# Kernel tuning notes

Measured on AMD Instinct MI355X. Metric: run time of the kernel, lower is better.

## Reference

```python
import jax, jax.numpy as jnp
import numpy as np
import math

# Module hyperparameters (match init_kwargs)
N_LEVELS = 16
LOG2_T = 19
T = 2 ** LOG2_T
BASE = (16, 16)
FINEST = (512, 512)
NUM_HASHGRID = 2
N_POINTS = 1_000_000
PRIME_Y = np.uint32(2654435761)  # standard NGP spatial-hash prime for the 2nd dim


def _resolutions():
    # replicate torch: int(base * b**i) per axis
    b_w = math.exp((math.log(FINEST[0]) - math.log(BASE[0])) / (N_LEVELS - 1))
    b_h = math.exp((math.log(FINEST[1]) - math.log(BASE[1])) / (N_LEVELS - 1))
    res_w = [int(BASE[0] * b_w ** i) for i in range(N_LEVELS)]
    res_h = [int(BASE[1] * b_h ** i) for i in range(N_LEVELS)]
    return jnp.array(np.stack([res_w, res_h], axis=-1), dtype=jnp.int32)  # [L,2]


def setup_inputs() -> dict:
    key = jax.random.key(0)
    k1, k2, k3 = jax.random.split(key, 3)
    x = jax.random.uniform(k1, (N_POINTS, 2), dtype=jnp.float32)
    hash_idxs = jax.random.randint(k2, (N_POINTS, 1), 0, NUM_HASHGRID, dtype=jnp.int32)
    # xavier-normal-like init of the hash tables [G, L, T, F]
    fan_in = N_LEVELS * T * 2
    fan_out = NUM_HASHGRID * T * 2
    std = math.sqrt(2.0 / (fan_in + fan_out))
    features = jax.random.normal(k3, (NUM_HASHGRID, N_LEVELS, T, 2), dtype=jnp.float32) * std
    return {"x": x, "features": features, "hash_idxs": hash_idxs}


def reference(x, features, hash_idxs):
    N = x.shape[0]
    res = _resolutions()                              # [L,2] int32
    scale = (res - 1).astype(jnp.float32)             # [L,2]
    pos = x[:, None, :] * scale[None]                 # [N,L,2]
    i0f = jnp.floor(pos)
    w = pos - i0f                                     # bilinear fractions [N,L,2]
    i0 = i0f.astype(jnp.int32).astype(jnp.uint32)     # [N,L,2]

    # 4 corner offsets: (0,0),(1,0),(0,1),(1,1)
    offs = jnp.array([[0, 0], [1, 0], [0, 1], [1, 1]], dtype=jnp.uint32)  # [4,2]
    corners = i0[:, :, None, :] + offs[None, None]    # [N,L,4,2]
    # NGP spatial hash, modulo table size via mask (T is power of 2)
    h = (corners[..., 0] ^ (corners[..., 1] * PRIME_Y)) & np.uint32(T - 1)  # [N,L,4]
    h = h.astype(jnp.int32)

    g = hash_idxs.reshape(-1)                         # [N] which hash grid
    lidx = jnp.arange(N_LEVELS, dtype=jnp.int32)
    feat = features[g[:, None, None], lidx[None, :, None], h]  # [N,L,4,2]

    wx, wy = w[..., 0], w[..., 1]
    wc = jnp.stack([(1 - wx) * (1 - wy), wx * (1 - wy), (1 - wx) * wy, wx * wy], axis=-1)  # [N,L,4]
    out = jnp.einsum('nlc,nlcf->nlf', wc, feat)       # [N,L,2]
    return out.reshape(N, N_LEVELS * 2)
```

## Files before the change

### kernel.cpp

```cpp
#include <hip/hip_runtime.h>
#include <math.h>

#define NL 16
#define TS (1u << 19)
#define TMASK (TS - 1u)
#define PRIME 2654435761u

#define NBINS 8192
#define BIN_GBIT 12
#define NCOPY 8

struct ScalePack { float s[NL]; };

__device__ __forceinline__ unsigned bin_of(float px, float py, int g) {
    int iy = (int)(py * 511.0f); iy = iy < 0 ? 0 : (iy > 511 ? 511 : iy);
    int ix = (int)(px * 511.0f); ix = ix < 0 ? 0 : (ix > 511 ? 511 : ix);
    return ((unsigned)g << BIN_GBIT) | ((unsigned)iy << 3) | ((unsigned)ix >> 6);
}

__global__ __launch_bounds__(256)
void k_zero(unsigned* __restrict__ p, int n) {
    int i = blockIdx.x * blockDim.x + threadIdx.x;
    if (i < n) p[i] = 0u;
}

__global__ __launch_bounds__(256)
void k_hist8(const float2* __restrict__ x, const int* __restrict__ hidx,
             unsigned* __restrict__ hist, int N)
{
    int n = blockIdx.x * 256 + threadIdx.x;
    if (n >= N) return;
    float2 p = x[n];
    unsigned b = bin_of(p.x, p.y, hidx[n]);
    unsigned c = (unsigned)blockIdx.x & (NCOPY - 1);
    atomicAdd(&hist[c * NBINS + b], 1u);
}

__global__ __launch_bounds__(1024)
void k_scan8(unsigned* __restrict__ hist)
{
    __shared__ unsigned part[1024];
    int t = threadIdx.x;
    int b0 = t * 8;

    unsigned s = 0;
    #pragma unroll
    for (int i = 0; i < 8; ++i) {
        int b = b0 + i;
        #pragma unroll
        for (int c = 0; c < NCOPY; ++c) s += hist[c * NBINS + b];
    }
    part[t] = s;
    __syncthreads();
    for (int d = 1; d < 1024; d <<= 1) {
        unsigned add = (t >= d) ? part[t - d] : 0u;
        __syncthreads();
        part[t] += add;
        __syncthreads();
    }
    unsigned running = t ? part[t - 1] : 0u;

    #pragma unroll
    for (int i = 0; i < 8; ++i) {
        int b = b0 + i;
        unsigned h[NCOPY];
        #pragma unroll
        for (int c = 0; c < NCOPY; ++c) h[c] = hist[c * NBINS + b];
        #pragma unroll
        for (int c = 0; c < NCOPY; ++c) {
            hist[c * NBINS + b] = running;
            running += h[c];
        }
    }
}

__global__ __launch_bounds__(256)
void k_scatter8(const float2* __restrict__ x, const int* __restrict__ hidx,
                unsigned* __restrict__ cur,
                float2* __restrict__ sxy, unsigned* __restrict__ smeta, int N)
{
    int n = blockIdx.x * 256 + threadIdx.x;
    if (n >= N) return;
    float2 p = x[n];
    int g = hidx[n];
    unsigned b = bin_of(p.x, p.y, g);
    unsigned c = (unsigned)blockIdx.x & (NCOPY - 1);
    unsigned pos = atomicAdd(&cur[c * NBINS + b], 1u);
    sxy[pos] = p;
    smeta[pos] = (unsigned)n | ((unsigned)g << 24);
}

__global__ __launch_bounds__(256)
void hashgrid2d_sorted(const float2* __restrict__ sxy,
                       const unsigned* __restrict__ smeta,
                       const float2* __restrict__ feat,
                       float4* __restrict__ out,
                       ScalePack sp, int N)
{
    int nwg = gridDim.x;
    int orig = blockIdx.x;
    int q = nwg >> 3, r = nwg & 7;
    int xcd = orig & 7, loc = orig >> 3;
    int bid = (xcd < r ? xcd * (q + 1) : r * (q + 1) + (xcd - r) * q) + loc;

    int n = bid * 256 + (int)threadIdx.x;
    if (n >= N) return;

    float2 p = sxy[n];
    unsigned meta = smeta[n];
    int g  = (int)(meta >> 24);
    int no = (int)(meta & 0xFFFFFFu);
    float px = p.x, py = p.y;
    const float2* fb = feat + (size_t)g * ((size_t)NL * TS);

    float of[2 * NL];

    #pragma unroll 4
    for (int l = 0; l < NL; ++l) {
        float s  = sp.s[l];
        float fx = px * s;
        float fy = py * s;
        float fx0 = floorf(fx), fy0 = floorf(fy);
        float wx = fx - fx0, wy = fy - fy0;
        unsigned ix = (unsigned)(int)fx0;
        unsigned iy = (unsigned)(int)fy0;
        unsigned hy0 = iy * PRIME;
        unsigned hy1 = (iy + 1u) * PRIME;

        const float2* tab = fb + (size_t)l * TS;
        float2 c00 = tab[( ix       ^ hy0) & TMASK];
        float2 c10 = tab[((ix + 1u) ^ hy0) & TMASK];
        float2 c01 = tab[( ix       ^ hy1) & TMASK];
        float2 c11 = tab[((ix + 1u) ^ hy1) & TMASK];

        float w00 = (1.f - wx) * (1.f - wy);
        float w10 = wx * (1.f - wy);
        float w01 = (1.f - wx) * wy;
        float w11 = wx * wy;

        of[2 * l]     = w00 * c00.x + w10 * c10.x + w01 * c01.x + w11 * c11.x;
        of[2 * l + 1] = w00 * c00.y + w10 * c10.y + w01 * c01.y + w11 * c11.y;
    }

    float4* op = out + (size_t)no * 8;
    #pragma unroll
    for (int qq = 0; qq < 8; ++qq)
        op[qq] = make_float4(of[4 * qq], of[4 * qq + 1], of[4 * qq + 2], of[4 * qq + 3]);
}

__global__ __launch_bounds__(256)
void hashgrid2d_fwd(const float2* __restrict__ x,
                    const float2* __restrict__ feat,
                    const int* __restrict__ hidx,
                    float4* __restrict__ out,
                    ScalePack sp, int N)
{
    int n = blockIdx.x * blockDim.x + threadIdx.x;
    if (n >= N) return;

    float2 p = x[n];
    float px = p.x, py = p.y;
    int g = hidx[n];
    const float2* fb = feat + (size_t)g * ((size_t)NL * TS);

    float of[2 * NL];

    #pragma unroll 4
    for (int l = 0; l < NL; ++l) {
        float s  = sp.s[l];
        float fx = px * s;
        float fy = py * s;
        float fx0 = floorf(fx), fy0 = floorf(fy);
        float wx = fx - fx0, wy = fy - fy0;
        unsigned ix = (unsigned)(int)fx0;
        unsigned iy = (unsigned)(int)fy0;
        unsigned hy0 = iy * PRIME;
        unsigned hy1 = (iy + 1u) * PRIME;

        const float2* tab = fb + (size_t)l * TS;
        float2 c00 = tab[( ix       ^ hy0) & TMASK];
        float2 c10 = tab[((ix + 1u) ^ hy0) & TMASK];
        float2 c01 = tab[( ix       ^ hy1) & TMASK];
        float2 c11 = tab[((ix + 1u) ^ hy1) & TMASK];

        float w00 = (1.f - wx) * (1.f - wy);
        float w10 = wx * (1.f - wy);
        float w01 = (1.f - wx) * wy;
        float w11 = wx * wy;

        of[2 * l]     = w00 * c00.x + w10 * c10.x + w01 * c01.x + w11 * c11.x;
        of[2 * l + 1] = w00 * c00.y + w10 * c10.y + w01 * c01.y + w11 * c11.y;
    }

    float4* op = out + (size_t)n * 8;
    #pragma unroll
    for (int qq = 0; qq < 8; ++qq)
        op[qq] = make_float4(of[4 * qq], of[4 * qq + 1], of[4 * qq + 2], of[4 * qq + 3]);
}

extern "C" void kernel_launch(void* const* d_in, const int* in_sizes, int n_in,
                              void* d_out, int out_size, void* d_ws, size_t ws_size,
                              hipStream_t stream) {
    const float2* x    = (const float2*)d_in[0];
    const float2* feat = (const float2*)d_in[1];
    const int*    hidx = (const int*)d_in[2];
    int N = in_sizes[0] / 2;

    ScalePack sp;
    double b = exp((log(512.0) - log(16.0)) / 15.0);
    for (int i = 0; i < NL; ++i) {
        int r = (int)(16.0 * pow(b, (double)i));
        sp.s[i] = (float)(r - 1);
    }

    int threads = 256;
    int blocks = (N + threads - 1) / threads;

    size_t curB  = (size_t)NCOPY * NBINS * 4;
    size_t xyB   = (size_t)N * 8;
    size_t metaB = (size_t)N * 4;
    size_t need  = curB + xyB + metaB;

    if (d_ws != nullptr && ws_size >= need && N < (1 << 24)) {
        unsigned* cur   = (unsigned*)d_ws;
        float2*   sxy   = (float2*)((char*)d_ws + curB);
        unsigned* smeta = (unsigned*)((char*)d_ws + curB + xyB);

        hipLaunchKernelGGL(k_zero, dim3((NCOPY * NBINS + 255) / 256), dim3(256), 0,
                           stream, cur, NCOPY * NBINS);
        hipLaunchKernelGGL(k_hist8, dim3(blocks), dim3(threads), 0, stream,
                           x, hidx, cur, N);
        hipLaunchKernelGGL(k_scan8, dim3(1), dim3(1024), 0, stream, cur);
        hipLaunchKernelGGL(k_scatter8, dim3(blocks), dim3(threads), 0, stream,
                           x, hidx, cur, sxy, smeta, N);
        hipLaunchKernelGGL(hashgrid2d_sorted, dim3(blocks), dim3(threads), 0, stream,
                           sxy, smeta, feat, (float4*)d_out, sp, N);
    } else {
        hipLaunchKernelGGL(hashgrid2d_fwd, dim3(blocks), dim3(threads), 0, stream,
                           x, feat, hidx, (float4*)d_out, sp, N);
    }
}
```

Measured before the change: 358.0 us.

## Replace global-atomic binning with per-block shared-memory histogram counting sort

Replaces the global-atomic histogram and scatter with a block-local LDS histogram over 256 persistent blocks, a per-bin column scan across blocks, and a global bin-base scan, followed by a scatter that uses LDS atomics. Bins are coarsened from 8192 to 4096. The aim is to cut contention on global atomics and drop the zeroing kernel. The cost is a larger workspace, an extra scan launch, and coarser bins, which may reduce locality in the table gathers. The old path is kept as a fallback when the workspace is too small.

After: 328.0 us. 8.4% less time.

```diff
diff --git a/kernel.cpp b/kernel.cpp
--- a/kernel.cpp
+++ b/kernel.cpp
@@ -6,16 +6,110 @@
 #define TMASK (TS - 1u)
 #define PRIME 2654435761u
 
-#define NBINS 8192
-#define BIN_GBIT 12
+#define SBINS 4096
+#define SBLK  256
+
+#define OBINS 8192
 #define NCOPY 8
 
 struct ScalePack { float s[NL]; };
 
-__device__ __forceinline__ unsigned bin_of(float px, float py, int g) {
+__device__ __forceinline__ unsigned bin4k_of(float px, float py, int g) {
     int iy = (int)(py * 511.0f); iy = iy < 0 ? 0 : (iy > 511 ? 511 : iy);
     int ix = (int)(px * 511.0f); ix = ix < 0 ? 0 : (ix > 511 ? 511 : ix);
-    return ((unsigned)g << BIN_GBIT) | ((unsigned)iy << 3) | ((unsigned)ix >> 6);
+    return ((unsigned)g << 11) | ((unsigned)iy << 2) | ((unsigned)ix >> 7);
+}
+
+__device__ __forceinline__ unsigned bin8k_of(float px, float py, int g) {
+    int iy = (int)(py * 511.0f); iy = iy < 0 ? 0 : (iy > 511 ? 511 : iy);
+    int ix = (int)(px * 511.0f); ix = ix < 0 ? 0 : (ix > 511 ? 511 : ix);
+    return ((unsigned)g << 12) | ((unsigned)iy << 3) | ((unsigned)ix >> 6);
+}
+
+
+__global__ __launch_bounds__(256)
+void k_hist_b(const float2* __restrict__ x, const int* __restrict__ hidx,
+              unsigned* __restrict__ H, int N)
+{
+    __shared__ unsigned lh[SBINS];
+    int t = threadIdx.x;
+    #pragma unroll
+    for (int i = t; i < SBINS; i += 256) lh[i] = 0u;
+    __syncthreads();
+
+    for (int n = blockIdx.x * 256 + t; n < N; n += SBLK * 256) {
+        float2 p = x[n];
+        atomicAdd(&lh[bin4k_of(p.x, p.y, hidx[n])], 1u);
+    }
+    __syncthreads();
+
+    unsigned* row = H + (size_t)blockIdx.x * SBINS;
+    #pragma unroll
+    for (int i = t; i < SBINS; i += 256) row[i] = lh[i];
+}
+
+__global__ __launch_bounds__(256)
+void k_s1(unsigned* __restrict__ H, unsigned* __restrict__ binTotal)
+{
+    __shared__ unsigned part[256];
+    int bin = blockIdx.x;
+    int t = threadIdx.x;
+    unsigned v = H[(size_t)t * SBINS + bin];
+    part[t] = v;
+    __syncthreads();
+    for (int d = 1; d < 256; d <<= 1) {
+        unsigned add = (t >= d) ? part[t - d] : 0u;
+        __syncthreads();
+        part[t] += add;
+        __syncthreads();
+    }
+    unsigned incl = part[t];
+    H[(size_t)t * SBINS + bin] = incl - v;
+    if (t == 255) binTotal[bin] = incl;
+}
+
+__global__ __launch_bounds__(1024)
+void k_s2(const unsigned* __restrict__ binTotal, unsigned* __restrict__ binBase)
+{
+    __shared__ unsigned part[1024];
+    int t = threadIdx.x;
+    unsigned v[4];
+    unsigned s = 0;
+    #pragma unroll
+    for (int i = 0; i < 4; ++i) { v[i] = binTotal[t * 4 + i]; s += v[i]; }
+    part[t] = s;
+    __syncthreads();
+    for (int d = 1; d < 1024; d <<= 1) {
+        unsigned add = (t >= d) ? part[t - d] : 0u;
+        __syncthreads();
+        part[t] += add;
+        __syncthreads();
+    }
+    unsigned base = t ? part[t - 1] : 0u;
+    #pragma unroll
+    for (int i = 0; i < 4; ++i) { binBase[t * 4 + i] = base; base += v[i]; }
+}
+
+__global__ __launch_bounds__(256)
+void k_scatter_b(const float2* __restrict__ x, const int* __restrict__ hidx,
+                 const unsigned* __restrict__ H, const unsigned* __restrict__ binBase,
+                 float2* __restrict__ sxy, unsigned* __restrict__ smeta, int N)
+{
+    __shared__ unsigned cur[SBINS];
+    int t = threadIdx.x;
+    const unsigned* row = H + (size_t)blockIdx.x * SBINS;
+    #pragma unroll
+    for (int i = t; i < SBINS; i += 256) cur[i] = binBase[i] + row[i];
+    __syncthreads();
+
+    for (int n = blockIdx.x * 256 + t; n < N; n += SBLK * 256) {
+        float2 p = x[n];
+        int g = hidx[n];
+        unsigned b = bin4k_of(p.x, p.y, g);
+        unsigned pos = atomicAdd(&cur[b], 1u);
+        sxy[pos] = p;
+        smeta[pos] = (unsigned)n | ((unsigned)g << 24);
+    }
 }
 
 __global__ __launch_bounds__(256)
@@ -31,9 +125,9 @@
     int n = blockIdx.x * 256 + threadIdx.x;
     if (n >= N) return;
     float2 p = x[n];
-    unsigned b = bin_of(p.x, p.y, hidx[n]);
+    unsigned b = bin8k_of(p.x, p.y, hidx[n]);
     unsigned c = (unsigned)blockIdx.x & (NCOPY - 1);
-    atomicAdd(&hist[c * NBINS + b], 1u);
+    atomicAdd(&hist[c * OBINS + b], 1u);
 }
 
 __global__ __launch_bounds__(1024)
@@ -42,13 +136,12 @@
     __shared__ unsigned part[1024];
     int t = threadIdx.x;
     int b0 = t * 8;
-
     unsigned s = 0;
     #pragma unroll
     for (int i = 0; i < 8; ++i) {
         int b = b0 + i;
         #pragma unroll
-        for (int c = 0; c < NCOPY; ++c) s += hist[c * NBINS + b];
+        for (int c = 0; c < NCOPY; ++c) s += hist[c * OBINS + b];
     }
     part[t] = s;
     __syncthreads();
@@ -59,16 +152,15 @@
         __syncthreads();
     }
     unsigned running = t ? part[t - 1] : 0u;
-
     #pragma unroll
     for (int i = 0; i < 8; ++i) {
         int b = b0 + i;
         unsigned h[NCOPY];
         #pragma unroll
-        for (int c = 0; c < NCOPY; ++c) h[c] = hist[c * NBINS + b];
+        for (int c = 0; c < NCOPY; ++c) h[c] = hist[c * OBINS + b];
         #pragma unroll
         for (int c = 0; c < NCOPY; ++c) {
-            hist[c * NBINS + b] = running;
+            hist[c * OBINS + b] = running;
             running += h[c];
         }
     }
@@ -83,9 +175,9 @@
     if (n >= N) return;
     float2 p = x[n];
     int g = hidx[n];
-    unsigned b = bin_of(p.x, p.y, g);
+    unsigned b = bin8k_of(p.x, p.y, g);
     unsigned c = (unsigned)blockIdx.x & (NCOPY - 1);
-    unsigned pos = atomicAdd(&cur[c * NBINS + b], 1u);
+    unsigned pos = atomicAdd(&cur[c * OBINS + b], 1u);
     sxy[pos] = p;
     smeta[pos] = (unsigned)n | ((unsigned)g << 24);
 }
@@ -216,18 +308,36 @@
     int threads = 256;
     int blocks = (N + threads - 1) / threads;
 
-    size_t curB  = (size_t)NCOPY * NBINS * 4;
     size_t xyB   = (size_t)N * 8;
     size_t metaB = (size_t)N * 4;
-    size_t need  = curB + xyB + metaB;
-
-    if (d_ws != nullptr && ws_size >= need && N < (1 << 24)) {
+
+    size_t HB       = (size_t)SBLK * SBINS * 4;
+    size_t need_new = HB + (size_t)SBINS * 4 * 2 + xyB + metaB;
+    size_t curB     = (size_t)NCOPY * OBINS * 4;
+    size_t need_old = curB + xyB + metaB;
+
+    if (d_ws != nullptr && ws_size >= need_new && N < (1 << 24)) {
+        unsigned* H        = (unsigned*)d_ws;
+        unsigned* binTotal = (unsigned*)((char*)d_ws + HB);
+        unsigned* binBase  = binTotal + SBINS;
+        float2*   sxy      = (float2*)((char*)d_ws + HB + (size_t)SBINS * 8);
+        unsigned* smeta    = (unsigned*)((char*)d_ws + HB + (size_t)SBINS * 8 + xyB);
+
+        hipLaunchKernelGGL(k_hist_b, dim3(SBLK), dim3(256), 0, stream,
+                           x, hidx, H, N);
+        hipLaunchKernelGGL(k_s1, dim3(SBINS), dim3(256), 0, stream, H, binTotal);
+        hipLaunchKernelGGL(k_s2, dim3(1), dim3(1024), 0, stream, binTotal, binBase);
+        hipLaunchKernelGGL(k_scatter_b, dim3(SBLK), dim3(256), 0, stream,
+                           x, hidx, H, binBase, sxy, smeta, N);
+        hipLaunchKernelGGL(hashgrid2d_sorted, dim3(blocks), dim3(threads), 0, stream,
+                           sxy, smeta, feat, (float4*)d_out, sp, N);
+    } else if (d_ws != nullptr && ws_size >= need_old && N < (1 << 24)) {
         unsigned* cur   = (unsigned*)d_ws;
         float2*   sxy   = (float2*)((char*)d_ws + curB);
         unsigned* smeta = (unsigned*)((char*)d_ws + curB + xyB);
 
-        hipLaunchKernelGGL(k_zero, dim3((NCOPY * NBINS + 255) / 256), dim3(256), 0,
-                           stream, cur, NCOPY * NBINS);
+        hipLaunchKernelGGL(k_zero, dim3((NCOPY * OBINS + 255) / 256), dim3(256), 0,
+                           stream, cur, NCOPY * OBINS);
         hipLaunchKernelGGL(k_hist8, dim3(blocks), dim3(threads), 0, stream,
                            x, hidx, cur, N);
         hipLaunchKernelGGL(k_scan8, dim3(1), dim3(1024), 0, stream, cur);
```
